# Kernel tuning notes

Hardware: AMD Instinct MI355X
Metric: run time of the kernel (lower is better)

## Reference

```python
import jax, jax.numpy as jnp
import numpy as np

DIM = 256
NUM_HEADS = 8
HEAD_DIM = DIM // NUM_HEADS


def setup_inputs() -> dict:
    key = jax.random.key(0)
    k1, k2, k3, k4 = jax.random.split(key, 4)
    b, n = 4, 2048
    x = jax.random.normal(k1, (b, n, DIM), dtype=jnp.float32)
    # Linear weights with fan-in scaling (matches nn.Linear init magnitude,
    # keeps exp(qk) numerically sane since the original has no max-subtraction).
    Wqkv = jax.random.normal(k2, (DIM, 3 * DIM), dtype=jnp.float32) * (DIM ** -0.5)
    Wout = jax.random.normal(k3, (DIM, DIM), dtype=jnp.float32) * (DIM ** -0.5)
    bout = jax.random.normal(k4, (DIM,), dtype=jnp.float32) * 0.01
    return {"x": x, "Wqkv": Wqkv, "Wout": Wout, "bout": bout}


def reference(x, Wqkv, Wout, bout):
    b, n, d = x.shape
    h, hd = NUM_HEADS, HEAD_DIM
    scale = hd ** -0.5
    qkv = x @ Wqkv  # [b, n, 3d]
    q, k, v = jnp.split(qkv, 3, axis=-1)
    # [b, h, n, hd]
    q = q.reshape(b, n, h, hd).transpose(0, 2, 1, 3) * scale
    k = k.reshape(b, n, h, hd).transpose(0, 2, 1, 3)
    v = v.reshape(b, n, h, hd).transpose(0, 2, 1, 3)
    # Original KeOps path: unnormalized exp (no max-subtraction), separate
    # numerator / denominator reductions, eps in denominator.
    scores = jnp.einsum('bhnd,bhmd->bhnm', q, k)  # [b, h, n, n]
    e = jnp.exp(scores)
    denom = jnp.sum(e, axis=-1, keepdims=True)          # [b, h, n, 1]
    numer = jnp.einsum('bhnm,bhmd->bhnd', e, v)         # [b, h, n, hd]
    out = numer / (denom + 1e-6)
    out = out.transpose(0, 2, 1, 3).reshape(b, n, d)
    return out @ Wout + bout
```

## Files before the change

### kernel.cpp

```cpp
#include <hip/hip_runtime.h>

#define DIM 256
#define NHEADS 8
#define HDIM 32

typedef _Float16 half8_t __attribute__((ext_vector_type(8)));
typedef _Float16 half4_t __attribute__((ext_vector_type(4)));
typedef float float4_t __attribute__((ext_vector_type(4)));

__device__ __forceinline__ float fast_exp2(float x) {
#if __has_builtin(__builtin_amdgcn_exp2f)
    return __builtin_amdgcn_exp2f(x);
#else
    return __expf(x * 0.6931471805599453f);
#endif
}

__device__ __forceinline__ void gload_lds16(const void* g, void* l) {
    __builtin_amdgcn_global_load_lds((const __attribute__((address_space(1))) void*)g,
                                     (__attribute__((address_space(3))) void*)l,
                                     16, 0, 0);
}

__global__ __launch_bounds__(256) void prep(const float* __restrict__ x,
                                            const float* __restrict__ Wqkv,
                                            const float* __restrict__ Wout,
                                            _Float16* __restrict__ xh,
                                            _Float16* __restrict__ WqT,
                                            _Float16* __restrict__ WoT) {
    __shared__ float ts[32][33];
    const int bid = blockIdx.x, t = threadIdx.x;
    if (bid < 1024) {
        size_t idx = (size_t)bid * 2048 + (size_t)t * 8;
        float tmp[8];
        *reinterpret_cast<float4*>(tmp)     = *reinterpret_cast<const float4*>(x + idx);
        *reinterpret_cast<float4*>(tmp + 4) = *reinterpret_cast<const float4*>(x + idx + 4);
        half8_t h;
        #pragma unroll
        for (int j = 0; j < 8; ++j) h[j] = (_Float16)tmp[j];
        *reinterpret_cast<half8_t*>(xh + idx) = h;
    } else {
        const float* src; _Float16* dst; int K, N, kb, nb;
        if (bid < 1024 + 192) { int b2 = bid - 1024; src = Wqkv; dst = WqT; K = 256; N = 768; nb = b2 % 24; kb = b2 / 24; }
        else                  { int b3 = bid - 1216; src = Wout; dst = WoT; K = 256; N = 256; nb = b3 % 8;  kb = b3 / 8; }
        const int tx = t & 31, ty = t >> 5;
        #pragma unroll
        for (int i = 0; i < 4; ++i) {
            int k = kb * 32 + ty + i * 8;
            ts[ty + i * 8][tx] = src[(size_t)k * N + nb * 32 + tx];
        }
        __syncthreads();
        #pragma unroll
        for (int i = 0; i < 4; ++i) {
            int nl = ty + i * 8;
            dst[(size_t)(nb * 32 + nl) * K + kb * 32 + tx] = (_Float16)ts[tx][nl];
        }
    }
}

template <bool OUT_HALF, bool VSPLIT, int MROWS>
__global__ __launch_bounds__(256) void gemm_h(const _Float16* __restrict__ A,
                                              const _Float16* __restrict__ BT,
                                              const float* __restrict__ bias,
                                              void* __restrict__ Cv,
                                              _Float16* __restrict__ VTo,
                                              int M, int N, int K, int ldc) {
    constexpr int BM = MROWS * 32;
    __shared__ alignas(16) _Float16 As[BM * 32];
    __shared__ alignas(16) _Float16 Bs[128 * 32];
    const int t = threadIdx.x, lane = t & 63, wave = t >> 6;
    const int l16 = lane & 15, quad = lane >> 4;
    const int m0 = blockIdx.y * BM, n0 = blockIdx.x * 128;
    const int wr = (wave >> 1) * (MROWS * 16), wc = (wave & 1) * 64;
    constexpr float QS = 0.17677669529663687f * 1.4426950408889634f;
    float4_t acc[MROWS][4];
    #pragma unroll
    for (int i = 0; i < MROWS; ++i)
        #pragma unroll
        for (int j = 0; j < 4; ++j) acc[i][j] = (float4_t){0.f, 0.f, 0.f, 0.f};

    const int srow = lane >> 2;
    const int scol = (lane & 3) * 8;

    for (int k0 = 0; k0 < K; k0 += 32) {
        #pragma unroll
        for (int i = 0; i < MROWS / 2; ++i) {
            int chunk = i * 4 + wave;
            int r = chunk * 16 + srow;
            gload_lds16(A + (size_t)(m0 + r) * K + k0 + scol, As + chunk * 512);
        }
        #pragma unroll
        for (int i = 0; i < 2; ++i) {
            int chunk = i * 4 + wave;
            int r = chunk * 16 + srow;
            gload_lds16(BT + (size_t)(n0 + r) * K + k0 + scol, Bs + chunk * 512);
        }
        __syncthreads();
        half8_t af[MROWS], bf[4];
        #pragma unroll
        for (int i = 0; i < MROWS; ++i)
            af[i] = *reinterpret_cast<const half8_t*>(As + (wr + i * 16 + l16) * 32 + quad * 8);
        #pragma unroll
        for (int j = 0; j < 4; ++j)
            bf[j] = *reinterpret_cast<const half8_t*>(Bs + (wc + j * 16 + l16) * 32 + quad * 8);
        #pragma unroll
        for (int i = 0; i < MROWS; ++i)
            #pragma unroll
            for (int j = 0; j < 4; ++j)
                acc[i][j] = __builtin_amdgcn_mfma_f32_16x16x32_f16(af[i], bf[j], acc[i][j], 0, 0, 0);
        __syncthreads();
    }

    if (VSPLIT && n0 >= 512) {
        const int bb = m0 >> 11;
        const int tok0 = (m0 & 2047) + wr;
        #pragma unroll
        for (int i = 0; i < MROWS; ++i)
            #pragma unroll
            for (int j = 0; j < 4; ++j) {
                int vcol = n0 + wc + j * 16 + l16 - 512;
                int hh = vcol >> 5, d = vcol & 31;
                half4_t p;
                #pragma unroll
                for (int r = 0; r < 4; ++r) p[r] = (_Float16)acc[i][j][r];
                *reinterpret_cast<half4_t*>(
                    VTo + ((size_t)(bb * NHEADS + hh) * HDIM + d) * 2048
                        + tok0 + i * 16 + quad * 4) = p;
            }
    } else {
        float bv[4] = {0.f, 0.f, 0.f, 0.f};
        if (bias != nullptr) {
            #pragma unroll
            for (int j = 0; j < 4; ++j) bv[j] = bias[n0 + wc + j * 16 + l16];
        }
        #pragma unroll
        for (int i = 0; i < MROWS; ++i)
            #pragma unroll
            for (int r = 0; r < 4; ++r) {
                int row = m0 + wr + i * 16 + quad * 4 + r;
                #pragma unroll
                for (int j = 0; j < 4; ++j) {
                    int col = n0 + wc + j * 16 + l16;
                    float v = acc[i][j][r] + bv[j];
                    if (VSPLIT && n0 < 256) v *= QS;
                    if (OUT_HALF) ((_Float16*)Cv)[(size_t)row * ldc + col] = (_Float16)v;
                    else          ((float*)Cv)[(size_t)row * ldc + col] = v;
                }
            }
    }
}


#define GLD(dst, addr) \
    asm volatile("global_load_dwordx4 %0, %1, off" : "=v"(dst) : "v"(addr))
#define WAITV(N) asm volatile("s_waitcnt vmcnt(" #N ")" ::: "memory")
#define SB0 __builtin_amdgcn_sched_barrier(0)

#define LOADASM(P, k0)                                            \
    do {                                                          \
        const _Float16* kp_ = kbase + (size_t)(k0) * 512;         \
        GLD(k##P[0], kp_);                                        \
        GLD(k##P[1], kp_ + (size_t)16 * 512);                     \
        GLD(k##P[2], kp_ + (size_t)32 * 512);                     \
        GLD(k##P[3], kp_ + (size_t)48 * 512);                     \
        const _Float16* vp_ = vbase + (k0);                       \
        GLD(v##P[0], vp_);                                        \
        GLD(v##P[1], vp_ + (size_t)16 * 2048);                    \
        GLD(v##P[2], vp_ + 32);                                   \
        GLD(v##P[3], vp_ + 32 + (size_t)16 * 2048);               \
    } while (0)

#define STEP(P)                                                                    \
    do {                                                                           \
        half4_t ep[4][4];                                                          \
        _Pragma("unroll")                                                          \
        for (int kb = 0; kb < 4; ++kb)                                             \
            _Pragma("unroll")                                                      \
            for (int g = 0; g < 4; ++g) {                                          \
                float4_t st = __builtin_amdgcn_mfma_f32_16x16x32_f16(              \
                    k##P[kb], qf[g], z, 0, 0, 0);                                  \
                auto lo = __builtin_amdgcn_cvt_pkrtz(fast_exp2(st[0]),             \
                                                     fast_exp2(st[1]));            \
                auto hi = __builtin_amdgcn_cvt_pkrtz(fast_exp2(st[2]),             \
                                                     fast_exp2(st[3]));            \
                ep[kb][g] = (half4_t){(_Float16)lo[0], (_Float16)lo[1],            \
                                      (_Float16)hi[0], (_Float16)hi[1]};           \
            }                                                                      \
        _Pragma("unroll")                                                          \
        for (int s = 0; s < 2; ++s) {                                              \
            _Pragma("unroll")                                                      \
            for (int tt = 0; tt < 2; ++tt)                                         \
                _Pragma("unroll")                                                  \
                for (int g = 0; g < 4; ++g)                                        \
                    *reinterpret_cast<half4_t*>(                                   \
                        esw + (g * 16 + l16) * 40 + tt * 16 + quad * 4) =          \
                        ep[s * 2 + tt][g];                                         \
            _Pragma("unroll")                                                      \
            for (int g = 0; g < 4; ++g) {                                          \
                half8_t ef = *reinterpret_cast<const half8_t*>(                    \
                    esw + (g * 16 + l16) * 40 + quad * 8);                         \
                num[g][0] = __builtin_amdgcn_mfma_f32_16x16x32_f16(                \
                    ef, v##P[s * 2], num[g][0], 0, 0, 0);                          \
                num[g][1] = __builtin_amdgcn_mfma_f32_16x16x32_f16(                \
                    ef, v##P[s * 2 + 1], num[g][1], 0, 0, 0);                      \
                dacc[g] = __builtin_amdgcn_mfma_f32_16x16x32_f16(                  \
                    ef, onef, dacc[g], 0, 0, 0);                                   \
            }                                                                      \
        }                                                                          \
    } while (0)

__global__ __launch_bounds__(256, 2) void attn_v11(const _Float16* __restrict__ qkh,
                                                   const _Float16* __restrict__ VT,
                                                   _Float16* __restrict__ NUM,
                                                   float* __restrict__ DEN) {
    __shared__ alignas(16) _Float16 es[4][64][40];
    const int bid = ((blockIdx.x & 7) << 6) | (blockIdx.x >> 3);
    const int kh = bid & 1;
    const int qb = (bid >> 1) & 7;
    const int bh = bid >> 4;
    const int b = bh >> 3, h = bh & 7;
    const int t = threadIdx.x, lane = t & 63, wave = t >> 6;
    const int l16 = lane & 15, quad = lane >> 4;
    const int bN = b * 2048;
    const int q0w = qb * 256 + wave * 64;
    const int kbeg = kh * 1024;

    const _Float16* kbase = qkh + (size_t)(bN + l16) * 512 + 256 + h * HDIM + quad * 8;
    const _Float16* vbase = VT + (size_t)bh * HDIM * 2048 + (size_t)l16 * 2048 + quad * 8;

    float4_t num[4][2];
    #pragma unroll
    for (int g = 0; g < 4; ++g)
        #pragma unroll
        for (int dt = 0; dt < 2; ++dt) num[g][dt] = (float4_t){0.f, 0.f, 0.f, 0.f};
    float4_t dacc[4];
    #pragma unroll
    for (int g = 0; g < 4; ++g) dacc[g] = (float4_t){0.f, 0.f, 0.f, 0.f};

    half8_t onef;
    #pragma unroll
    for (int j = 0; j < 8; ++j) onef[j] = (_Float16)1.0f;

    _Float16* esw = &es[wave][0][0];
    const float4_t z = {0.f, 0.f, 0.f, 0.f};

    half8_t qf[4];
    {
        const _Float16* qrow = qkh + (size_t)(bN + q0w + l16) * 512 + h * HDIM + quad * 8;
        GLD(qf[0], qrow);
        GLD(qf[1], qrow + (size_t)16 * 512);
        GLD(qf[2], qrow + (size_t)32 * 512);
        GLD(qf[3], qrow + (size_t)48 * 512);
    }

    half8_t kA[4], vA[4], kB[4], vB[4];
    LOADASM(A, kbeg);
    for (int k0 = kbeg; k0 < kbeg + 1024; k0 += 128) {
        LOADASM(B, k0 + 64);
        WAITV(8);
        SB0;
        STEP(A);
        if (k0 + 128 < kbeg + 1024) {
            LOADASM(A, k0 + 128);
            WAITV(8);
        } else {
            WAITV(0);
        }
        SB0;
        STEP(B);
    }

    _Float16* ob = NUM + (size_t)kh * 2097152 + (size_t)(bN + q0w) * DIM + h * HDIM;
    #pragma unroll
    for (int g = 0; g < 4; ++g)
        #pragma unroll
        for (int r = 0; r < 4; ++r) {
            size_t ro = (size_t)(g * 16 + quad * 4 + r) * DIM;
            ob[ro + l16]      = (_Float16)num[g][0][r];
            ob[ro + 16 + l16] = (_Float16)num[g][1][r];
        }
    if (l16 == 0) {
        #pragma unroll
        for (int g = 0; g < 4; ++g)
            #pragma unroll
            for (int r = 0; r < 4; ++r)
                DEN[kh * 65536 + bh * 2048 + q0w + g * 16 + quad * 4 + r] = dacc[g][r];
    }
}

__global__ __launch_bounds__(256) void combine(const _Float16* __restrict__ NUM,
                                               const float* __restrict__ DEN,
                                               _Float16* __restrict__ attnh) {
    const size_t idx = ((size_t)blockIdx.x * 256 + threadIdx.x) * 8;
    const int row = (int)(idx >> 8);
    const int c = (int)(idx & 255);
    const int b = row >> 11, tok = row & 2047, h = c >> 5;
    const int di = (b * 8 + h) * 2048 + tok;
    float rcp = 1.0f / (DEN[di] + DEN[di + 65536] + 1e-6f);
    half8_t n0 = *reinterpret_cast<const half8_t*>(NUM + idx);
    half8_t n1 = *reinterpret_cast<const half8_t*>(NUM + idx + 2097152);
    *reinterpret_cast<half8_t*>(attnh + idx) = (n0 + n1) * (_Float16)rcp;
}

extern "C" void kernel_launch(void* const* d_in, const int* in_sizes, int n_in,
                              void* d_out, int out_size, void* d_ws, size_t ws_size,
                              hipStream_t stream) {
    const float* x    = (const float*)d_in[0];
    const float* Wqkv = (const float*)d_in[1];
    const float* Wout = (const float*)d_in[2];
    const float* bout = (const float*)d_in[3];
    float* out = (float*)d_out;
    const int M = 8192;

    _Float16* xh    = (_Float16*)d_ws;
    _Float16* WqT   = xh + (size_t)M * DIM;
    _Float16* WoT   = WqT + 768 * 256;
    _Float16* qkh   = WoT + 256 * 256;
    _Float16* vt    = qkh + (size_t)M * 512;
    _Float16* NUM   = vt + (size_t)32 * HDIM * 2048;
    float*    DEN   = (float*)(NUM + (size_t)2 * M * DIM);
    _Float16* attnh = (_Float16*)(DEN + 2 * 65536);

    hipLaunchKernelGGL(prep, dim3(1280), dim3(256), 0, stream, x, Wqkv, Wout, xh, WqT, WoT);
    hipLaunchKernelGGL((gemm_h<true, true, 2>), dim3(6, 128), dim3(256), 0, stream,
                       xh, WqT, (const float*)nullptr, (void*)qkh, vt, M, 768, DIM, 512);
    hipLaunchKernelGGL(attn_v11, dim3(512), dim3(256), 0, stream, qkh, vt, NUM, DEN);
    hipLaunchKernelGGL(combine, dim3(1024), dim3(256), 0, stream, NUM, DEN, attnh);
    hipLaunchKernelGGL((gemm_h<false, false, 2>), dim3(2, 128), dim3(256), 0, stream,
                       attnh, WoT, bout, (void*)out, (_Float16*)nullptr, M, DIM, DIM, DIM);
}
```

Measured before the change: 120.8 us.

## Fuse split-K combine into output GEMM and raise priority around attention MFMA steps

Removes the separate combine kernel. The output projection GEMM now loads both split-K numerator halves and the denominators, normalizes them, and writes the A tile to LDS itself. This avoids one launch and a round trip of the normalized attention output through global memory. In exchange, each K iteration uses synchronous loads instead of async LDS loads, and the two numerator tiles are read again for each of the two N-column blocks. It also wraps the attention compute steps in s_setprio so the waves doing MFMA work get scheduled first, and specializes the QKV GEMM template into a plain kernel.

Result: no change. 121.4 us (median of 2 runs) (+0.5%).

```diff
diff --git a/kernel.cpp b/kernel.cpp
--- a/kernel.cpp
+++ b/kernel.cpp
@@ -58,24 +58,21 @@
     }
 }
 
-template <bool OUT_HALF, bool VSPLIT, int MROWS>
-__global__ __launch_bounds__(256) void gemm_h(const _Float16* __restrict__ A,
-                                              const _Float16* __restrict__ BT,
-                                              const float* __restrict__ bias,
-                                              void* __restrict__ Cv,
-                                              _Float16* __restrict__ VTo,
-                                              int M, int N, int K, int ldc) {
-    constexpr int BM = MROWS * 32;
-    __shared__ alignas(16) _Float16 As[BM * 32];
+__global__ __launch_bounds__(256) void gemm_qkv(const _Float16* __restrict__ A,
+                                                const _Float16* __restrict__ BT,
+                                                _Float16* __restrict__ Cv,
+                                                _Float16* __restrict__ VTo) {
+    constexpr int K = 256, ldc = 512;
+    __shared__ alignas(16) _Float16 As[64 * 32];
     __shared__ alignas(16) _Float16 Bs[128 * 32];
     const int t = threadIdx.x, lane = t & 63, wave = t >> 6;
     const int l16 = lane & 15, quad = lane >> 4;
-    const int m0 = blockIdx.y * BM, n0 = blockIdx.x * 128;
-    const int wr = (wave >> 1) * (MROWS * 16), wc = (wave & 1) * 64;
+    const int m0 = blockIdx.y * 64, n0 = blockIdx.x * 128;
+    const int wr = (wave >> 1) * 32, wc = (wave & 1) * 64;
     constexpr float QS = 0.17677669529663687f * 1.4426950408889634f;
-    float4_t acc[MROWS][4];
-    #pragma unroll
-    for (int i = 0; i < MROWS; ++i)
+    float4_t acc[2][4];
+    #pragma unroll
+    for (int i = 0; i < 2; ++i)
         #pragma unroll
         for (int j = 0; j < 4; ++j) acc[i][j] = (float4_t){0.f, 0.f, 0.f, 0.f};
 
@@ -83,9 +80,8 @@
     const int scol = (lane & 3) * 8;
 
     for (int k0 = 0; k0 < K; k0 += 32) {
-        #pragma unroll
-        for (int i = 0; i < MROWS / 2; ++i) {
-            int chunk = i * 4 + wave;
+        {
+            int chunk = wave;
             int r = chunk * 16 + srow;
             gload_lds16(A + (size_t)(m0 + r) * K + k0 + scol, As + chunk * 512);
         }
@@ -96,26 +92,26 @@
             gload_lds16(BT + (size_t)(n0 + r) * K + k0 + scol, Bs + chunk * 512);
         }
         __syncthreads();
-        half8_t af[MROWS], bf[4];
-        #pragma unroll
-        for (int i = 0; i < MROWS; ++i)
+        half8_t af[2], bf[4];
+        #pragma unroll
+        for (int i = 0; i < 2; ++i)
             af[i] = *reinterpret_cast<const half8_t*>(As + (wr + i * 16 + l16) * 32 + quad * 8);
         #pragma unroll
         for (int j = 0; j < 4; ++j)
             bf[j] = *reinterpret_cast<const half8_t*>(Bs + (wc + j * 16 + l16) * 32 + quad * 8);
         #pragma unroll
-        for (int i = 0; i < MROWS; ++i)
+        for (int i = 0; i < 2; ++i)
             #pragma unroll
             for (int j = 0; j < 4; ++j)
                 acc[i][j] = __builtin_amdgcn_mfma_f32_16x16x32_f16(af[i], bf[j], acc[i][j], 0, 0, 0);
         __syncthreads();
     }
 
-    if (VSPLIT && n0 >= 512) {
+    if (n0 >= 512) {
         const int bb = m0 >> 11;
         const int tok0 = (m0 & 2047) + wr;
         #pragma unroll
-        for (int i = 0; i < MROWS; ++i)
+        for (int i = 0; i < 2; ++i)
             #pragma unroll
             for (int j = 0; j < 4; ++j) {
                 int vcol = n0 + wc + j * 16 + l16 - 512;
@@ -128,23 +124,17 @@
                         + tok0 + i * 16 + quad * 4) = p;
             }
     } else {
-        float bv[4] = {0.f, 0.f, 0.f, 0.f};
-        if (bias != nullptr) {
-            #pragma unroll
-            for (int j = 0; j < 4; ++j) bv[j] = bias[n0 + wc + j * 16 + l16];
-        }
-        #pragma unroll
-        for (int i = 0; i < MROWS; ++i)
+        #pragma unroll
+        for (int i = 0; i < 2; ++i)
             #pragma unroll
             for (int r = 0; r < 4; ++r) {
                 int row = m0 + wr + i * 16 + quad * 4 + r;
                 #pragma unroll
                 for (int j = 0; j < 4; ++j) {
                     int col = n0 + wc + j * 16 + l16;
-                    float v = acc[i][j][r] + bv[j];
-                    if (VSPLIT && n0 < 256) v *= QS;
-                    if (OUT_HALF) ((_Float16*)Cv)[(size_t)row * ldc + col] = (_Float16)v;
-                    else          ((float*)Cv)[(size_t)row * ldc + col] = v;
+                    float v = acc[i][j][r];
+                    if (n0 < 256) v *= QS;
+                    Cv[(size_t)row * ldc + col] = (_Float16)v;
                 }
             }
     }
@@ -259,7 +249,9 @@
         LOADASM(B, k0 + 64);
         WAITV(8);
         SB0;
+        __builtin_amdgcn_s_setprio(1);
         STEP(A);
+        __builtin_amdgcn_s_setprio(0);
         if (k0 + 128 < kbeg + 1024) {
             LOADASM(A, k0 + 128);
             WAITV(8);
@@ -267,7 +259,9 @@
             WAITV(0);
         }
         SB0;
+        __builtin_amdgcn_s_setprio(1);
         STEP(B);
+        __builtin_amdgcn_s_setprio(0);
     }
 
     _Float16* ob = NUM + (size_t)kh * 2097152 + (size_t)(bN + q0w) * DIM + h * HDIM;
@@ -288,18 +282,78 @@
     }
 }
 
-__global__ __launch_bounds__(256) void combine(const _Float16* __restrict__ NUM,
-                                               const float* __restrict__ DEN,
-                                               _Float16* __restrict__ attnh) {
-    const size_t idx = ((size_t)blockIdx.x * 256 + threadIdx.x) * 8;
-    const int row = (int)(idx >> 8);
-    const int c = (int)(idx & 255);
-    const int b = row >> 11, tok = row & 2047, h = c >> 5;
-    const int di = (b * 8 + h) * 2048 + tok;
-    float rcp = 1.0f / (DEN[di] + DEN[di + 65536] + 1e-6f);
-    half8_t n0 = *reinterpret_cast<const half8_t*>(NUM + idx);
-    half8_t n1 = *reinterpret_cast<const half8_t*>(NUM + idx + 2097152);
-    *reinterpret_cast<half8_t*>(attnh + idx) = (n0 + n1) * (_Float16)rcp;
+__global__ __launch_bounds__(256) void gemm_out(const _Float16* __restrict__ NUM,
+                                                const float* __restrict__ DEN,
+                                                const _Float16* __restrict__ BT,
+                                                const float* __restrict__ bias,
+                                                float* __restrict__ C) {
+    constexpr int K = 256;
+    __shared__ alignas(16) _Float16 As[64 * 32];
+    __shared__ alignas(16) _Float16 Bs[128 * 32];
+    const int t = threadIdx.x, lane = t & 63, wave = t >> 6;
+    const int l16 = lane & 15, quad = lane >> 4;
+    const int m0 = blockIdx.y * 64, n0 = blockIdx.x * 128;
+    const int wr = (wave >> 1) * 32, wc = (wave & 1) * 64;
+    float4_t acc[2][4];
+    #pragma unroll
+    for (int i = 0; i < 2; ++i)
+        #pragma unroll
+        for (int j = 0; j < 4; ++j) acc[i][j] = (float4_t){0.f, 0.f, 0.f, 0.f};
+
+    const int srow = lane >> 2;
+    const int scol = (lane & 3) * 8;
+    const int ar = t >> 2;
+    const int ac = (t & 3) * 8;
+    const int row = m0 + ar;
+    const int bb = row >> 11, tok = row & 2047;
+
+    for (int k0 = 0; k0 < K; k0 += 32) {
+        {
+            const int h = k0 >> 5;
+            const int di = (bb * 8 + h) * 2048 + tok;
+            float den = DEN[di] + DEN[di + 65536] + 1e-6f;
+            _Float16 rcp = (_Float16)(1.0f / den);
+            size_t idx = (size_t)row * 256 + k0 + ac;
+            half8_t nu0 = *reinterpret_cast<const half8_t*>(NUM + idx);
+            half8_t nu1 = *reinterpret_cast<const half8_t*>(NUM + idx + 2097152);
+            *reinterpret_cast<half8_t*>(As + ar * 32 + ac) = (nu0 + nu1) * rcp;
+        }
+        #pragma unroll
+        for (int i = 0; i < 2; ++i) {
+            int chunk = i * 4 + wave;
+            int r = chunk * 16 + srow;
+            gload_lds16(BT + (size_t)(n0 + r) * K + k0 + scol, Bs + chunk * 512);
+        }
+        __syncthreads();
+        half8_t af[2], bf[4];
+        #pragma unroll
+        for (int i = 0; i < 2; ++i)
+            af[i] = *reinterpret_cast<const half8_t*>(As + (wr + i * 16 + l16) * 32 + quad * 8);
+        #pragma unroll
+        for (int j = 0; j < 4; ++j)
+            bf[j] = *reinterpret_cast<const half8_t*>(Bs + (wc + j * 16 + l16) * 32 + quad * 8);
+        #pragma unroll
+        for (int i = 0; i < 2; ++i)
+            #pragma unroll
+            for (int j = 0; j < 4; ++j)
+                acc[i][j] = __builtin_amdgcn_mfma_f32_16x16x32_f16(af[i], bf[j], acc[i][j], 0, 0, 0);
+        __syncthreads();
+    }
+
+    float bv[4];
+    #pragma unroll
+    for (int j = 0; j < 4; ++j) bv[j] = bias[n0 + wc + j * 16 + l16];
+    #pragma unroll
+    for (int i = 0; i < 2; ++i)
+        #pragma unroll
+        for (int r = 0; r < 4; ++r) {
+            int orow = m0 + wr + i * 16 + quad * 4 + r;
+            #pragma unroll
+            for (int j = 0; j < 4; ++j) {
+                int col = n0 + wc + j * 16 + l16;
+                C[(size_t)orow * DIM + col] = acc[i][j][r] + bv[j];
+            }
+        }
 }
 
 extern "C" void kernel_launch(void* const* d_in, const int* in_sizes, int n_in,
@@ -319,13 +373,10 @@
     _Float16* vt    = qkh + (size_t)M * 512;
     _Float16* NUM   = vt + (size_t)32 * HDIM * 2048;
     float*    DEN   = (float*)(NUM + (size_t)2 * M * DIM);
-    _Float16* attnh = (_Float16*)(DEN + 2 * 65536);
 
     hipLaunchKernelGGL(prep, dim3(1280), dim3(256), 0, stream, x, Wqkv, Wout, xh, WqT, WoT);
-    hipLaunchKernelGGL((gemm_h<true, true, 2>), dim3(6, 128), dim3(256), 0, stream,
-                       xh, WqT, (const float*)nullptr, (void*)qkh, vt, M, 768, DIM, 512);
+    hipLaunchKernelGGL(gemm_qkv, dim3(6, 128), dim3(256), 0, stream, xh, WqT, qkh, vt);
     hipLaunchKernelGGL(attn_v11, dim3(512), dim3(256), 0, stream, qkh, vt, NUM, DEN);
-    hipLaunchKernelGGL(combine, dim3(1024), dim3(256), 0, stream, NUM, DEN, attnh);
-    hipLaunchKernelGGL((gemm_h<false, false, 2>), dim3(2, 128), dim3(256), 0, stream,
-                       attnh, WoT, bout, (void*)out, (_Float16*)nullptr, M, DIM, DIM, DIM);
-}
+    hipLaunchKernelGGL(gemm_out, dim3(2, 128), dim3(256), 0, stream,
+                       NUM, DEN, WoT, bout, out);
+}
```
